# Optimization experiments

Hardware: AMD Instinct MI355X
Metric: run time of the kernel (lower is better)

The kernel has to match this reference:

```python
import jax, jax.numpy as jnp
import numpy as np

N_NODES = 200_000
N_UND = 3_200_000        # undirected masked edges
E = 2 * N_UND            # directed edges


def _seg_mean(m, dst, n_nodes):
    # DGL fn.mean: mean over incoming edge messages; zero-in-degree nodes get 0.
    s = jax.ops.segment_sum(m, dst, num_segments=n_nodes)
    deg = jax.ops.segment_sum(jnp.ones((m.shape[0], 1), m.dtype), dst, num_segments=n_nodes)
    return s / jnp.maximum(deg, 1.0)


def setup_inputs() -> dict:
    key = jax.random.key(0)
    ks = jax.random.split(key, 18)
    w = lambda k, s: jax.random.normal(k, s, dtype=jnp.float32) * 0.1
    return {
        'node_feat': jax.random.normal(ks[0], (N_NODES, 7), dtype=jnp.float32),
        'edge_feat': jax.random.normal(ks[1], (E, 4), dtype=jnp.float32),
        'edge_mask': jax.random.normal(ks[2], (N_UND, 1), dtype=jnp.float32),
        'src': jax.random.randint(ks[3], (E,), 0, N_NODES),
        'dst': jax.random.randint(ks[4], (E,), 0, N_NODES),
        'W1a': w(ks[5], (11, 32)), 'b1a': jnp.zeros((32,), jnp.float32),
        'W1b': w(ks[6], (32, 32)), 'b1b': jnp.zeros((32,), jnp.float32),
        'W2a': w(ks[7], (32, 32)), 'b2a': jnp.zeros((32,), jnp.float32),
        'W2b': w(ks[8], (32, 32)), 'b2b': jnp.zeros((32,), jnp.float32),
        'Wm1': w(ks[9], (32, 16)), 'bm1': jnp.zeros((16,), jnp.float32),
        'Wm2': w(ks[10], (16, 2)), 'bm2': jnp.zeros((2,), jnp.float32),
    }


def reference(node_feat, edge_feat, edge_mask, src, dst,
              W1a, b1a, W1b, b1b, W2a, b2a, W2b, b2b, Wm1, bm1, Wm2, bm2):
    n_nodes = node_feat.shape[0]
    relu = jax.nn.relu
    # interleave mask to both edge directions: [m0, m0, m1, m1, ...]
    m_full = jax.nn.sigmoid(jnp.repeat(edge_mask, 2, axis=0))  # [E, 1]
    # layer 1: masked cat(edge_h, src_h) -> mean over dst -> MLP
    msg1 = m_full * jnp.concatenate([edge_feat, node_feat[src]], axis=1)  # [E, 11]
    h = _seg_mean(msg1, dst, n_nodes)                                      # [N, 11]
    h = relu(relu(h @ W1a + b1a) @ W1b + b1b)                              # [N, 32]
    # layer 2: masked src_h -> mean over dst -> MLP
    msg2 = m_full * h[src]                                                 # [E, 32]
    h = _seg_mean(msg2, dst, n_nodes)                                      # [N, 32]
    h = relu(relu(h @ W2a + b2a) @ W2b + b2b)                              # [N, 32]
    # global max pool + readout MLP + softmax (batch_size=1 path)
    g = jnp.max(h, axis=0)                                                 # [32]
    logits = relu(g @ Wm1 + bm1) @ Wm2 + bm2                               # [2]
    return jax.nn.softmax(logits)[None, :]                                 # [1, 2]
```

## Files before the change

kernel.cpp:

```cpp
#include <hip/hip_runtime.h>
#include <hip/hip_fp16.h>
#include <math.h>

#define SCHUNK 1024
#define PMAX   80
#define BSHIFT 9
#define MAXBKT 1024
#define BINB   1024
#define EPT    8

__device__ __forceinline__ float sigmoidf_(float x) {
    return 1.0f / (1.0f + __expf(-x));
}

union I2H { int i; __half2 h; };
__device__ __forceinline__ int pack_h2(float a, float b) {
    I2H u; u.h = __floats2half2_rn(a, b); return u.i;
}
__device__ __forceinline__ float2 unpack_h2(int w) {
    I2H u; u.i = w; return __half22float2(u.h);
}

typedef int v4i_nt __attribute__((ext_vector_type(4)));
typedef float v4f_nt __attribute__((ext_vector_type(4)));
__device__ __forceinline__ int4 ldnt16(const int4* p) {
    v4i_nt v = __builtin_nontemporal_load((const v4i_nt*)p);
    return make_int4(v[0], v[1], v[2], v[3]);
}
__device__ __forceinline__ float4 ldnt16f(const float* p) {
    v4f_nt v = __builtin_nontemporal_load((const v4f_nt*)p);
    return make_float4(v[0], v[1], v[2], v[3]);
}

__global__ void hist_rank(const int* __restrict__ dst, int* __restrict__ deg,
                          int* __restrict__ rank, int E) {
    int e = blockIdx.x * blockDim.x + threadIdx.x;
    if (e < E) rank[e] = atomicAdd(&deg[dst[e]], 1);
}

__global__ void scan_part(const int* __restrict__ deg, int* __restrict__ bsum, int N) {
    __shared__ int tot[256];
    int t = threadIdx.x;
    int base = blockIdx.x * SCHUNK + t * 4;
    int s = 0;
    if (base + 3 < N) {
        int4 v = *(const int4*)(deg + base);
        s = v.x + v.y + v.z + v.w;
    } else {
#pragma unroll
        for (int j = 0; j < 4; ++j) if (base + j < N) s += deg[base + j];
    }
    tot[t] = s;
    __syncthreads();
    for (int o = 128; o >= 1; o >>= 1) {
        if (t < o) tot[t] += tot[t + o];
        __syncthreads();
    }
    if (t == 0) bsum[blockIdx.x] = tot[0];
}

__global__ void scan_mid(int* __restrict__ bsum, int* __restrict__ off, int B, int N) {
    __shared__ int tmp[256];
    int t = threadIdx.x;
    int chunk = (B + 255) / 256;
    int lo = t * chunk, hi = min(lo + chunk, B);
    int s = 0;
    for (int i = lo; i < hi; ++i) s += bsum[i];
    tmp[t] = s;
    __syncthreads();
    for (int o = 1; o < 256; o <<= 1) {
        int v = (t >= o) ? tmp[t - o] : 0;
        __syncthreads();
        tmp[t] += v;
        __syncthreads();
    }
    int run = (t == 0) ? 0 : tmp[t - 1];
    for (int i = lo; i < hi; ++i) { int d = bsum[i]; bsum[i] = run; run += d; }
    if (t == 255) off[N] = tmp[255];
}

__global__ void scan_fin(const int* __restrict__ deg, const int* __restrict__ bsum,
                         int* __restrict__ off, int N) {
    __shared__ int tots[256];
    int t = threadIdx.x;
    int base = blockIdx.x * SCHUNK + t * 4;
    int v0 = 0, v1 = 0, v2 = 0, v3 = 0;
    if (base + 3 < N) {
        int4 v = *(const int4*)(deg + base);
        v0 = v.x; v1 = v.y; v2 = v.z; v3 = v.w;
    } else {
        if (base + 0 < N) v0 = deg[base + 0];
        if (base + 1 < N) v1 = deg[base + 1];
        if (base + 2 < N) v2 = deg[base + 2];
        if (base + 3 < N) v3 = deg[base + 3];
    }
    tots[t] = v0 + v1 + v2 + v3;
    __syncthreads();
    for (int o = 1; o < 256; o <<= 1) {
        int v = (t >= o) ? tots[t - o] : 0;
        __syncthreads();
        tots[t] += v;
        __syncthreads();
    }
    int run = bsum[blockIdx.x] + ((t == 0) ? 0 : tots[t - 1]);
    if (base + 0 < N) off[base + 0] = run; run += v0;
    if (base + 1 < N) off[base + 1] = run; run += v1;
    if (base + 2 < N) off[base + 2] = run; run += v2;
    if (base + 3 < N) off[base + 3] = run;
}

__global__ void pack_nodes(const float* __restrict__ nf, int4* __restrict__ nf16, int N) {
    int n = blockIdx.x * blockDim.x + threadIdx.x;
    if (n >= N) return;
    const float* p = nf + (size_t)n * 7;
    int4 w;
    w.x = pack_h2(p[0], p[1]);
    w.y = pack_h2(p[2], p[3]);
    w.z = pack_h2(p[4], p[5]);
    w.w = pack_h2(p[6], 0.0f);
    nf16[n] = w;
}

__global__ __launch_bounds__(BINB)
void binA(const int* __restrict__ dst, const int* __restrict__ src,
          const float* __restrict__ edge_mask, const float* __restrict__ edge_feat,
          const float* __restrict__ node_feat,
          int* __restrict__ bktCnt, int4* __restrict__ region, int4* __restrict__ nf16,
          int E, int N, int nbkt, int bcap) {
    __shared__ int cnt[MAXBKT];
    __shared__ int base[MAXBKT];
    int t = threadIdx.x;
    int gt = blockIdx.x * BINB + t;
    if (gt < N) {
        const float* p = node_feat + (size_t)gt * 7;
        int4 w;
        w.x = pack_h2(p[0], p[1]);
        w.y = pack_h2(p[2], p[3]);
        w.z = pack_h2(p[4], p[5]);
        w.w = pack_h2(p[6], 0.0f);
        nf16[gt] = w;
    }
    for (int i = t; i < nbkt; i += BINB) cnt[i] = 0;
    __syncthreads();
    int4 rec[EPT];
    int  bl[EPT];
    int e0 = blockIdx.x * (BINB * EPT) + t;
#pragma unroll
    for (int j = 0; j < EPT; ++j) {
        int e = e0 + j * BINB;
        bl[j] = -1;
        if (e < E) {
            int d = dst[e];
            int s = src[e];
            float m = sigmoidf_(edge_mask[e >> 1]);
            float4 ef = ldnt16f(edge_feat + (size_t)e * 4);
            int b = d >> BSHIFT;
            int dlo = d & ((1 << BSHIFT) - 1);
            int lr = atomicAdd(&cnt[b], 1);
            rec[j].x = (dlo << 18) | s;
            rec[j].y = pack_h2(m * ef.x, m * ef.y);
            rec[j].z = pack_h2(m * ef.z, m * ef.w);
            rec[j].w = __float_as_int(m);
            bl[j] = (b << 16) | lr;
        }
    }
    __syncthreads();
    for (int i = t; i < nbkt; i += BINB)
        base[i] = atomicAdd(&bktCnt[i], cnt[i]);
    __syncthreads();
#pragma unroll
    for (int j = 0; j < EPT; ++j) {
        if (bl[j] >= 0) {
            int b = bl[j] >> 16, lr = bl[j] & 0xffff;
            int pos = base[b] + lr;
            if (pos < bcap) region[(size_t)b * bcap + pos] = rec[j];
        }
    }
}

__global__ __launch_bounds__(1024)
void fillS(const int4* __restrict__ region, const int* __restrict__ bktCnt,
           int4* __restrict__ recP, int* __restrict__ deg, int N, int bcap) {
    __shared__ int cnt[1 << BSHIFT];
    int b = blockIdx.x;
    int t = threadIdx.x;
    if (t < (1 << BSHIFT)) cnt[t] = 0;
    __syncthreads();
    int count = min(bktCnt[b], bcap);
    const int4* reg = region + (size_t)b * bcap;
    int n0 = b << BSHIFT;
    for (int i = t; i < count; i += blockDim.x) {
        int4 w = ldnt16(reg + i);
        int dlo = ((unsigned)w.x) >> 18;
        int r = atomicAdd(&cnt[dlo], 1);
        if (r < PMAX) {
            w.x &= 0x3FFFF;
            recP[(size_t)(n0 + dlo) * PMAX + r] = w;
        }
    }
    __syncthreads();
    if (t < (1 << BSHIFT) && n0 + t < N) deg[n0 + t] = cnt[t];
}

__global__ void hist_fill_p(const int* __restrict__ dst, const int* __restrict__ src,
                            const float* __restrict__ edge_mask,
                            const float* __restrict__ edge_feat,
                            const float* __restrict__ node_feat,
                            int* __restrict__ deg, int4* __restrict__ recP,
                            int4* __restrict__ nf16, int E, int N) {
    int t = blockIdx.x * blockDim.x + threadIdx.x;
    if (t < N) {
        const float* p = node_feat + (size_t)t * 7;
        int4 w;
        w.x = pack_h2(p[0], p[1]);
        w.y = pack_h2(p[2], p[3]);
        w.z = pack_h2(p[4], p[5]);
        w.w = pack_h2(p[6], 0.0f);
        nf16[t] = w;
    }
    int e0 = blockIdx.x * (blockDim.x << 2) + threadIdx.x;
    int e1 = e0 + blockDim.x;
    int e2 = e1 + blockDim.x;
    int e3 = e2 + blockDim.x;
    bool v0 = e0 < E, v1 = e1 < E, v2 = e2 < E, v3 = e3 < E;
    int d0 = 0, d1 = 0, d2 = 0, d3 = 0;
    int s0 = 0, s1 = 0, s2 = 0, s3 = 0;
    float k0 = 0, k1 = 0, k2 = 0, k3 = 0;
    float4 f0 = {}, f1 = {}, f2 = {}, f3 = {};
    if (v0) { d0 = dst[e0]; s0 = src[e0]; k0 = edge_mask[e0 >> 1]; f0 = ldnt16f(edge_feat + (size_t)e0 * 4); }
    if (v1) { d1 = dst[e1]; s1 = src[e1]; k1 = edge_mask[e1 >> 1]; f1 = ldnt16f(edge_feat + (size_t)e1 * 4); }
    if (v2) { d2 = dst[e2]; s2 = src[e2]; k2 = edge_mask[e2 >> 1]; f2 = ldnt16f(edge_feat + (size_t)e2 * 4); }
    if (v3) { d3 = dst[e3]; s3 = src[e3]; k3 = edge_mask[e3 >> 1]; f3 = ldnt16f(edge_feat + (size_t)e3 * 4); }
    float m0 = sigmoidf_(k0), m1 = sigmoidf_(k1), m2 = sigmoidf_(k2), m3 = sigmoidf_(k3);
    int4 w0, w1, w2, w3;
    w0.x = s0; w0.y = pack_h2(m0 * f0.x, m0 * f0.y); w0.z = pack_h2(m0 * f0.z, m0 * f0.w); w0.w = __float_as_int(m0);
    w1.x = s1; w1.y = pack_h2(m1 * f1.x, m1 * f1.y); w1.z = pack_h2(m1 * f1.z, m1 * f1.w); w1.w = __float_as_int(m1);
    w2.x = s2; w2.y = pack_h2(m2 * f2.x, m2 * f2.y); w2.z = pack_h2(m2 * f2.z, m2 * f2.w); w2.w = __float_as_int(m2);
    w3.x = s3; w3.y = pack_h2(m3 * f3.x, m3 * f3.y); w3.z = pack_h2(m3 * f3.z, m3 * f3.w); w3.w = __float_as_int(m3);
    int r0 = 0, r1 = 0, r2 = 0, r3 = 0;
    if (v0) r0 = atomicAdd(&deg[d0], 1);
    if (v1) r1 = atomicAdd(&deg[d1], 1);
    if (v2) r2 = atomicAdd(&deg[d2], 1);
    if (v3) r3 = atomicAdd(&deg[d3], 1);
    if (v0 && r0 < PMAX) recP[(size_t)d0 * PMAX + r0] = w0;
    if (v1 && r1 < PMAX) recP[(size_t)d1 * PMAX + r1] = w1;
    if (v2 && r2 < PMAX) recP[(size_t)d2 * PMAX + r2] = w2;
    if (v3 && r3 < PMAX) recP[(size_t)d3 * PMAX + r3] = w3;
}

__global__ void agg1_p(const int4* __restrict__ recP, const int* __restrict__ degv,
                       const int4* __restrict__ nf16,
                       const float* __restrict__ W1a, const float* __restrict__ b1a,
                       const float* __restrict__ W1b, const float* __restrict__ b1b,
                       __half* __restrict__ h1h, int N) {
    __shared__ float sW1a[11 * 32], sb1a[32], sW1b[32 * 32], sb1b[32];
    for (int i = threadIdx.x; i < 11 * 32; i += blockDim.x) sW1a[i] = W1a[i];
    for (int i = threadIdx.x; i < 32 * 32; i += blockDim.x) sW1b[i] = W1b[i];
    if (threadIdx.x < 32) { sb1a[threadIdx.x] = b1a[threadIdx.x]; sb1b[threadIdx.x] = b1b[threadIdx.x]; }
    __syncthreads();
    int n = blockIdx.x * (blockDim.x >> 2) + (threadIdx.x >> 2);
    int sub = threadIdx.x & 3;
    int deg = 0;
    size_t start = 0;
    if (n < N) { deg = degv[n]; start = (size_t)n * PMAX; }
    int dd = min(deg, PMAX);
    float x[11];
#pragma unroll
    for (int j = 0; j < 11; ++j) x[j] = 0.0f;
    int i = sub;
    for (; i + 4 < dd; i += 8) {
        int4 r0 = ldnt16(recP + start + i);
        int4 r1 = ldnt16(recP + start + i + 4);
        int4 nw0 = nf16[r0.x];
        int4 nw1 = nf16[r1.x];
        {
            float m = __int_as_float(r0.w);
            float2 e01 = unpack_h2(r0.y), e23 = unpack_h2(r0.z);
            x[0] += e01.x; x[1] += e01.y; x[2] += e23.x; x[3] += e23.y;
            float2 n01 = unpack_h2(nw0.x), n23 = unpack_h2(nw0.y);
            float2 n45 = unpack_h2(nw0.z), n6 = unpack_h2(nw0.w);
            x[4] += m * n01.x; x[5]  += m * n01.y; x[6] += m * n23.x; x[7] += m * n23.y;
            x[8] += m * n45.x; x[9]  += m * n45.y; x[10] += m * n6.x;
        }
        {
            float m = __int_as_float(r1.w);
            float2 e01 = unpack_h2(r1.y), e23 = unpack_h2(r1.z);
            x[0] += e01.x; x[1] += e01.y; x[2] += e23.x; x[3] += e23.y;
            float2 n01 = unpack_h2(nw1.x), n23 = unpack_h2(nw1.y);
            float2 n45 = unpack_h2(nw1.z), n6 = unpack_h2(nw1.w);
            x[4] += m * n01.x; x[5]  += m * n01.y; x[6] += m * n23.x; x[7] += m * n23.y;
            x[8] += m * n45.x; x[9]  += m * n45.y; x[10] += m * n6.x;
        }
    }
    for (; i < dd; i += 4) {
        int4 r = ldnt16(recP + start + i);
        float m = __int_as_float(r.w);
        float2 e01 = unpack_h2(r.y), e23 = unpack_h2(r.z);
        x[0] += e01.x; x[1] += e01.y; x[2] += e23.x; x[3] += e23.y;
        int4 nw = nf16[r.x];
        float2 n01 = unpack_h2(nw.x), n23 = unpack_h2(nw.y);
        float2 n45 = unpack_h2(nw.z), n6 = unpack_h2(nw.w);
        x[4] += m * n01.x; x[5]  += m * n01.y; x[6] += m * n23.x; x[7] += m * n23.y;
        x[8] += m * n45.x; x[9]  += m * n45.y; x[10] += m * n6.x;
    }
#pragma unroll
    for (int j = 0; j < 11; ++j) {
        x[j] += __shfl_xor(x[j], 1);
        x[j] += __shfl_xor(x[j], 2);
    }
    if (n >= N) return;
    float inv = 1.0f / fmaxf((float)deg, 1.0f);
#pragma unroll
    for (int j = 0; j < 11; ++j) x[j] *= inv;
    float hdn[32];
#pragma unroll
    for (int k = 0; k < 32; ++k) {
        float acc = sb1a[k];
#pragma unroll
        for (int j = 0; j < 11; ++j) acc += x[j] * sW1a[j * 32 + k];
        hdn[k] = fmaxf(acc, 0.0f);
    }
    float o[32];
#pragma unroll
    for (int k2 = 0; k2 < 32; ++k2) {
        float acc = sb1b[k2];
#pragma unroll
        for (int k = 0; k < 32; ++k) acc += hdn[k] * sW1b[k * 32 + k2];
        o[k2] = fmaxf(acc, 0.0f);
    }
    int4 w;
    w.x = pack_h2(o[8 * sub + 0], o[8 * sub + 1]);
    w.y = pack_h2(o[8 * sub + 2], o[8 * sub + 3]);
    w.z = pack_h2(o[8 * sub + 4], o[8 * sub + 5]);
    w.w = pack_h2(o[8 * sub + 6], o[8 * sub + 7]);
    ((int4*)(h1h + (size_t)n * 32))[sub] = w;
}

__global__ void agg2_p(const int4* __restrict__ recP, const int* __restrict__ degv,
                       const __half* __restrict__ h1h,
                       const float* __restrict__ W2a, const float* __restrict__ b2a,
                       const float* __restrict__ W2b, const float* __restrict__ b2b,
                       float* __restrict__ gmax, int N) {
    __shared__ float sW2a[32 * 32], sb2a[32], sW2b[32 * 32], sb2b[32];
    __shared__ int smax[32];
    for (int i = threadIdx.x; i < 32 * 32; i += blockDim.x) { sW2a[i] = W2a[i]; sW2b[i] = W2b[i]; }
    if (threadIdx.x < 32) {
        sb2a[threadIdx.x] = b2a[threadIdx.x];
        sb2b[threadIdx.x] = b2b[threadIdx.x];
        smax[threadIdx.x] = 0;
    }
    __syncthreads();
    int n = blockIdx.x * (blockDim.x >> 2) + (threadIdx.x >> 2);
    int sub = threadIdx.x & 3;
    bool valid = (n < N);
    int deg = 0;
    size_t start = 0;
    if (valid) { deg = degv[n]; start = (size_t)n * PMAX; }
    int dd = min(deg, PMAX);
    float x[32];
#pragma unroll
    for (int j = 0; j < 32; ++j) x[j] = 0.0f;
    int i = sub;
    for (; i + 4 < dd; i += 8) {
        int4 r0 = ldnt16(recP + start + i);
        int4 r1 = ldnt16(recP + start + i + 4);
        const int4* hp0 = (const int4*)(h1h + (size_t)r0.x * 32);
        const int4* hp1 = (const int4*)(h1h + (size_t)r1.x * 32);
        int4 g00 = hp0[0], g01 = hp0[1], g02 = hp0[2], g03 = hp0[3];
        int4 g10 = hp1[0], g11 = hp1[1], g12 = hp1[2], g13 = hp1[3];
        {
            float m = __int_as_float(r0.w);
            float2 a, b, c, d;
            a = unpack_h2(g00.x); b = unpack_h2(g00.y); c = unpack_h2(g00.z); d = unpack_h2(g00.w);
            x[0] += m * a.x; x[1] += m * a.y; x[2] += m * b.x; x[3] += m * b.y;
            x[4] += m * c.x; x[5] += m * c.y; x[6] += m * d.x; x[7] += m * d.y;
            a = unpack_h2(g01.x); b = unpack_h2(g01.y); c = unpack_h2(g01.z); d = unpack_h2(g01.w);
            x[8] += m * a.x; x[9] += m * a.y; x[10] += m * b.x; x[11] += m * b.y;
            x[12] += m * c.x; x[13] += m * c.y; x[14] += m * d.x; x[15] += m * d.y;
            a = unpack_h2(g02.x); b = unpack_h2(g02.y); c = unpack_h2(g02.z); d = unpack_h2(g02.w);
            x[16] += m * a.x; x[17] += m * a.y; x[18] += m * b.x; x[19] += m * b.y;
            x[20] += m * c.x; x[21] += m * c.y; x[22] += m * d.x; x[23] += m * d.y;
            a = unpack_h2(g03.x); b = unpack_h2(g03.y); c = unpack_h2(g03.z); d = unpack_h2(g03.w);
            x[24] += m * a.x; x[25] += m * a.y; x[26] += m * b.x; x[27] += m * b.y;
            x[28] += m * c.x; x[29] += m * c.y; x[30] += m * d.x; x[31] += m * d.y;
        }
        {
            float m = __int_as_float(r1.w);
            float2 a, b, c, d;
            a = unpack_h2(g10.x); b = unpack_h2(g10.y); c = unpack_h2(g10.z); d = unpack_h2(g10.w);
            x[0] += m * a.x; x[1] += m * a.y; x[2] += m * b.x; x[3] += m * b.y;
            x[4] += m * c.x; x[5] += m * c.y; x[6] += m * d.x; x[7] += m * d.y;
            a = unpack_h2(g11.x); b = unpack_h2(g11.y); c = unpack_h2(g11.z); d = unpack_h2(g11.w);
            x[8] += m * a.x; x[9] += m * a.y; x[10] += m * b.x; x[11] += m * b.y;
            x[12] += m * c.x; x[13] += m * c.y; x[14] += m * d.x; x[15] += m * d.y;
            a = unpack_h2(g12.x); b = unpack_h2(g12.y); c = unpack_h2(g12.z); d = unpack_h2(g12.w);
            x[16] += m * a.x; x[17] += m * a.y; x[18] += m * b.x; x[19] += m * b.y;
            x[20] += m * c.x; x[21] += m * c.y; x[22] += m * d.x; x[23] += m * d.y;
            a = unpack_h2(g13.x); b = unpack_h2(g13.y); c = unpack_h2(g13.z); d = unpack_h2(g13.w);
            x[24] += m * a.x; x[25] += m * a.y; x[26] += m * b.x; x[27] += m * b.y;
            x[28] += m * c.x; x[29] += m * c.y; x[30] += m * d.x; x[31] += m * d.y;
        }
    }
    for (; i < dd; i += 4) {
        int4 r = ldnt16(recP + start + i);
        float m = __int_as_float(r.w);
        const int4* hp = (const int4*)(h1h + (size_t)r.x * 32);
#pragma unroll
        for (int q = 0; q < 4; ++q) {
            int4 v = hp[q];
            float2 a = unpack_h2(v.x), b = unpack_h2(v.y);
            float2 c = unpack_h2(v.z), d = unpack_h2(v.w);
            x[8 * q + 0] += m * a.x; x[8 * q + 1] += m * a.y;
            x[8 * q + 2] += m * b.x; x[8 * q + 3] += m * b.y;
            x[8 * q + 4] += m * c.x; x[8 * q + 5] += m * c.y;
            x[8 * q + 6] += m * d.x; x[8 * q + 7] += m * d.y;
        }
    }
#pragma unroll
    for (int j = 0; j < 32; ++j) {
        x[j] += __shfl_xor(x[j], 1);
        x[j] += __shfl_xor(x[j], 2);
    }
    float inv = 1.0f / fmaxf((float)deg, 1.0f);
#pragma unroll
    for (int j = 0; j < 32; ++j) x[j] *= inv;
    float hdn[32];
#pragma unroll
    for (int k = 0; k < 32; ++k) {
        float acc = sb2a[k];
#pragma unroll
        for (int j = 0; j < 32; ++j) acc += x[j] * sW2a[j * 32 + k];
        hdn[k] = fmaxf(acc, 0.0f);
    }
    int lane = threadIdx.x & 63;
#pragma unroll
    for (int k2 = 0; k2 < 32; ++k2) {
        float acc = sb2b[k2];
#pragma unroll
        for (int k = 0; k < 32; ++k) acc += hdn[k] * sW2b[k * 32 + k2];
        float v = valid ? fmaxf(acc, 0.0f) : 0.0f;
#pragma unroll
        for (int o = 32; o >= 1; o >>= 1)
            v = fmaxf(v, __shfl_xor(v, o));
        if (lane == 0) atomicMax(&smax[k2], __float_as_int(v));
    }
    __syncthreads();
    if (threadIdx.x < 32) atomicMax((int*)&gmax[threadIdx.x], smax[threadIdx.x]);
}

__global__ void fill_rec16(const int* __restrict__ dst, const int* __restrict__ rank,
                           const int* __restrict__ off,
                           const float* __restrict__ edge_mask,
                           const int* __restrict__ src,
                           const float* __restrict__ edge_feat,
                           int4* __restrict__ rec, int E) {
    int e = blockIdx.x * blockDim.x + threadIdx.x;
    if (e >= E) return;
    int p = off[dst[e]] + rank[e];
    float m = sigmoidf_(edge_mask[e >> 1]);
    float4 ef = ldnt16f(edge_feat + (size_t)e * 4);
    int4 w;
    w.x = src[e];
    w.y = pack_h2(m * ef.x, m * ef.y);
    w.z = pack_h2(m * ef.z, m * ef.w);
    w.w = __float_as_int(m);
    rec[p] = w;
}

__global__ void agg1_16(const int4* __restrict__ rec, const int* __restrict__ off,
                        const int4* __restrict__ nf16,
                        const float* __restrict__ W1a, const float* __restrict__ b1a,
                        const float* __restrict__ W1b, const float* __restrict__ b1b,
                        __half* __restrict__ h1h, int N) {
    __shared__ float sW1a[11 * 32], sb1a[32], sW1b[32 * 32], sb1b[32];
    for (int i = threadIdx.x; i < 11 * 32; i += blockDim.x) sW1a[i] = W1a[i];
    for (int i = threadIdx.x; i < 32 * 32; i += blockDim.x) sW1b[i] = W1b[i];
    if (threadIdx.x < 32) { sb1a[threadIdx.x] = b1a[threadIdx.x]; sb1b[threadIdx.x] = b1b[threadIdx.x]; }
    __syncthreads();
    int n = blockIdx.x * (blockDim.x >> 2) + (threadIdx.x >> 2);
    int sub = threadIdx.x & 3;
    int start = 0, deg = 0;
    if (n < N) { start = off[n]; deg = off[n + 1] - start; }
    float x[11];
#pragma unroll
    for (int j = 0; j < 11; ++j) x[j] = 0.0f;
    for (int i = sub; i < deg; i += 4) {
        int4 r = ldnt16(rec + start + i);
        float m = __int_as_float(r.w);
        float2 e01 = unpack_h2(r.y), e23 = unpack_h2(r.z);
        x[0] += e01.x; x[1] += e01.y; x[2] += e23.x; x[3] += e23.y;
        int4 nw = nf16[r.x];
        float2 n01 = unpack_h2(nw.x), n23 = unpack_h2(nw.y);
        float2 n45 = unpack_h2(nw.z), n6 = unpack_h2(nw.w);
        x[4] += m * n01.x; x[5]  += m * n01.y; x[6] += m * n23.x; x[7] += m * n23.y;
        x[8] += m * n45.x; x[9]  += m * n45.y; x[10] += m * n6.x;
    }
#pragma unroll
    for (int j = 0; j < 11; ++j) {
        x[j] += __shfl_xor(x[j], 1);
        x[j] += __shfl_xor(x[j], 2);
    }
    if (n >= N) return;
    float inv = 1.0f / fmaxf((float)deg, 1.0f);
#pragma unroll
    for (int j = 0; j < 11; ++j) x[j] *= inv;
    float hdn[32];
#pragma unroll
    for (int k = 0; k < 32; ++k) {
        float acc = sb1a[k];
#pragma unroll
        for (int j = 0; j < 11; ++j) acc += x[j] * sW1a[j * 32 + k];
        hdn[k] = fmaxf(acc, 0.0f);
    }
    float o[32];
#pragma unroll
    for (int k2 = 0; k2 < 32; ++k2) {
        float acc = sb1b[k2];
#pragma unroll
        for (int k = 0; k < 32; ++k) acc += hdn[k] * sW1b[k * 32 + k2];
        o[k2] = fmaxf(acc, 0.0f);
    }
    int4 w;
    w.x = pack_h2(o[8 * sub + 0], o[8 * sub + 1]);
    w.y = pack_h2(o[8 * sub + 2], o[8 * sub + 3]);
    w.z = pack_h2(o[8 * sub + 4], o[8 * sub + 5]);
    w.w = pack_h2(o[8 * sub + 6], o[8 * sub + 7]);
    ((int4*)(h1h + (size_t)n * 32))[sub] = w;
}

__global__ void agg2_16(const int4* __restrict__ rec, const int* __restrict__ off,
                        const __half* __restrict__ h1h,
                        const float* __restrict__ W2a, const float* __restrict__ b2a,
                        const float* __restrict__ W2b, const float* __restrict__ b2b,
                        float* __restrict__ gmax, int N) {
    __shared__ float sW2a[32 * 32], sb2a[32], sW2b[32 * 32], sb2b[32];
    __shared__ int smax[32];
    for (int i = threadIdx.x; i < 32 * 32; i += blockDim.x) { sW2a[i] = W2a[i]; sW2b[i] = W2b[i]; }
    if (threadIdx.x < 32) {
        sb2a[threadIdx.x] = b2a[threadIdx.x];
        sb2b[threadIdx.x] = b2b[threadIdx.x];
        smax[threadIdx.x] = 0;
    }
    __syncthreads();
    int n = blockIdx.x * (blockDim.x >> 2) + (threadIdx.x >> 2);
    int sub = threadIdx.x & 3;
    bool valid = (n < N);
    int start = 0, deg = 0;
    if (valid) { start = off[n]; deg = off[n + 1] - start; }
    float x[32];
#pragma unroll
    for (int j = 0; j < 32; ++j) x[j] = 0.0f;
    for (int i = sub; i < deg; i += 4) {
        int4 r = ldnt16(rec + start + i);
        float m = __int_as_float(r.w);
        const int4* hp = (const int4*)(h1h + (size_t)r.x * 32);
#pragma unroll
        for (int q = 0; q < 4; ++q) {
            int4 v = hp[q];
            float2 a = unpack_h2(v.x), b = unpack_h2(v.y);
            float2 c = unpack_h2(v.z), d = unpack_h2(v.w);
            x[8 * q + 0] += m * a.x; x[8 * q + 1] += m * a.y;
            x[8 * q + 2] += m * b.x; x[8 * q + 3] += m * b.y;
            x[8 * q + 4] += m * c.x; x[8 * q + 5] += m * c.y;
            x[8 * q + 6] += m * d.x; x[8 * q + 7] += m * d.y;
        }
    }
#pragma unroll
    for (int j = 0; j < 32; ++j) {
        x[j] += __shfl_xor(x[j], 1);
        x[j] += __shfl_xor(x[j], 2);
    }
    float inv = 1.0f / fmaxf((float)deg, 1.0f);
#pragma unroll
    for (int j = 0; j < 32; ++j) x[j] *= inv;
    float hdn[32];
#pragma unroll
    for (int k = 0; k < 32; ++k) {
        float acc = sb2a[k];
#pragma unroll
        for (int j = 0; j < 32; ++j) acc += x[j] * sW2a[j * 32 + k];
        hdn[k] = fmaxf(acc, 0.0f);
    }
    int lane = threadIdx.x & 63;
#pragma unroll
    for (int k2 = 0; k2 < 32; ++k2) {
        float acc = sb2b[k2];
#pragma unroll
        for (int k = 0; k < 32; ++k) acc += hdn[k] * sW2b[k * 32 + k2];
        float v = valid ? fmaxf(acc, 0.0f) : 0.0f;
#pragma unroll
        for (int o = 32; o >= 1; o >>= 1)
            v = fmaxf(v, __shfl_xor(v, o));
        if (lane == 0) atomicMax(&smax[k2], __float_as_int(v));
    }
    __syncthreads();
    if (threadIdx.x < 32) atomicMax((int*)&gmax[threadIdx.x], smax[threadIdx.x]);
}

__global__ void fill_rec(const int* __restrict__ dst, const int* __restrict__ rank,
                         const int* __restrict__ off,
                         const float* __restrict__ edge_mask,
                         const int* __restrict__ src,
                         int2* __restrict__ rec, int E) {
    int e = blockIdx.x * blockDim.x + threadIdx.x;
    if (e >= E) return;
    int p = off[dst[e]] + rank[e];
    float m = sigmoidf_(edge_mask[e >> 1]);
    int mq = (int)(m * 16384.0f + 0.5f);
    mq = min(mq, 16383);
    unsigned packed = ((unsigned)src[e] << 14) | (unsigned)mq;
    rec[p] = make_int2(e, (int)packed);
}

__global__ void agg1_rec(const int2* __restrict__ rec, const int* __restrict__ off,
                         const float* __restrict__ edge_feat,
                         const float* __restrict__ node_feat,
                         const float* __restrict__ W1a, const float* __restrict__ b1a,
                         const float* __restrict__ W1b, const float* __restrict__ b1b,
                         float* __restrict__ h1, int N) {
    __shared__ float sW1a[11 * 32], sb1a[32], sW1b[32 * 32], sb1b[32];
    for (int i = threadIdx.x; i < 11 * 32; i += blockDim.x) sW1a[i] = W1a[i];
    for (int i = threadIdx.x; i < 32 * 32; i += blockDim.x) sW1b[i] = W1b[i];
    if (threadIdx.x < 32) { sb1a[threadIdx.x] = b1a[threadIdx.x]; sb1b[threadIdx.x] = b1b[threadIdx.x]; }
    __syncthreads();
    int n = blockIdx.x * blockDim.x + threadIdx.x;
    if (n >= N) return;
    int start = off[n];
    int deg = off[n + 1] - start;
    float x[11];
#pragma unroll
    for (int j = 0; j < 11; ++j) x[j] = 0.0f;
    for (int i = 0; i < deg; ++i) {
        int2 r = rec[start + i];
        int e = r.x;
        unsigned packed = (unsigned)r.y;
        int s = (int)(packed >> 14);
        float m = (float)(packed & 16383u) * (1.0f / 16384.0f);
        float4 ef = *(const float4*)(edge_feat + (size_t)e * 4);
        x[0] += m * ef.x; x[1] += m * ef.y; x[2] += m * ef.z; x[3] += m * ef.w;
        const float* nf = node_feat + (size_t)s * 7;
#pragma unroll
        for (int j = 0; j < 7; ++j) x[4 + j] += m * nf[j];
    }
    float inv = 1.0f / fmaxf((float)deg, 1.0f);
#pragma unroll
    for (int j = 0; j < 11; ++j) x[j] *= inv;
    float hdn[32];
#pragma unroll
    for (int k = 0; k < 32; ++k) {
        float acc = sb1a[k];
#pragma unroll
        for (int j = 0; j < 11; ++j) acc += x[j] * sW1a[j * 32 + k];
        hdn[k] = fmaxf(acc, 0.0f);
    }
    float o[32];
#pragma unroll
    for (int k2 = 0; k2 < 32; ++k2) {
        float acc = sb1b[k2];
#pragma unroll
        for (int k = 0; k < 32; ++k) acc += hdn[k] * sW1b[k * 32 + k2];
        o[k2] = fmaxf(acc, 0.0f);
    }
    float4* outp = (float4*)(h1 + (size_t)n * 32);
#pragma unroll
    for (int q = 0; q < 8; ++q)
        outp[q] = make_float4(o[4 * q], o[4 * q + 1], o[4 * q + 2], o[4 * q + 3]);
}

__global__ void agg2_rec(const int2* __restrict__ rec, const int* __restrict__ off,
                         const float* __restrict__ h1,
                         const float* __restrict__ W2a, const float* __restrict__ b2a,
                         const float* __restrict__ W2b, const float* __restrict__ b2b,
                         float* __restrict__ gmax, int N) {
    __shared__ float sW2a[32 * 32], sb2a[32], sW2b[32 * 32], sb2b[32];
    __shared__ int smax[32];
    for (int i = threadIdx.x; i < 32 * 32; i += blockDim.x) { sW2a[i] = W2a[i]; sW2b[i] = W2b[i]; }
    if (threadIdx.x < 32) {
        sb2a[threadIdx.x] = b2a[threadIdx.x];
        sb2b[threadIdx.x] = b2b[threadIdx.x];
        smax[threadIdx.x] = 0;
    }
    __syncthreads();
    int n = blockIdx.x * blockDim.x + threadIdx.x;
    bool valid = (n < N);
    int nn = valid ? n : 0;
    int start = valid ? off[nn] : 0;
    int deg = valid ? (off[nn + 1] - start) : 0;
    float x[32];
#pragma unroll
    for (int j = 0; j < 32; ++j) x[j] = 0.0f;
    for (int i = 0; i < deg; ++i) {
        int2 r = rec[start + i];
        unsigned packed = (unsigned)r.y;
        int s = (int)(packed >> 14);
        float m = (float)(packed & 16383u) * (1.0f / 16384.0f);
        const float4* hp = (const float4*)(h1 + (size_t)s * 32);
#pragma unroll
        for (int q = 0; q < 8; ++q) {
            float4 v = hp[q];
            x[4 * q + 0] += m * v.x;
            x[4 * q + 1] += m * v.y;
            x[4 * q + 2] += m * v.z;
            x[4 * q + 3] += m * v.w;
        }
    }
    float inv = 1.0f / fmaxf((float)deg, 1.0f);
#pragma unroll
    for (int j = 0; j < 32; ++j) x[j] *= inv;
    float hdn[32];
#pragma unroll
    for (int k = 0; k < 32; ++k) {
        float acc = sb2a[k];
#pragma unroll
        for (int j = 0; j < 32; ++j) acc += x[j] * sW2a[j * 32 + k];
        hdn[k] = fmaxf(acc, 0.0f);
    }
    int lane = threadIdx.x & 63;
#pragma unroll
    for (int k2 = 0; k2 < 32; ++k2) {
        float acc = sb2b[k2];
#pragma unroll
        for (int k = 0; k < 32; ++k) acc += hdn[k] * sW2b[k * 32 + k2];
        float v = valid ? fmaxf(acc, 0.0f) : 0.0f;
#pragma unroll
        for (int o = 32; o >= 1; o >>= 1)
            v = fmaxf(v, __shfl_xor(v, o));
        if (lane == 0) atomicMax(&smax[k2], __float_as_int(v));
    }
    __syncthreads();
    if (threadIdx.x < 32) atomicMax((int*)&gmax[threadIdx.x], smax[threadIdx.x]);
}

__global__ void readout(const float* __restrict__ gmax,
                        const float* __restrict__ Wm1, const float* __restrict__ bm1,
                        const float* __restrict__ Wm2, const float* __restrict__ bm2,
                        float* __restrict__ out) {
    __shared__ float p[16];
    int t = threadIdx.x;
    if (t < 16) {
        float acc = bm1[t];
        for (int j = 0; j < 32; ++j) acc += gmax[j] * Wm1[j * 16 + t];
        p[t] = fmaxf(acc, 0.0f);
    }
    __syncthreads();
    if (t == 0) {
        float l0 = bm2[0], l1 = bm2[1];
        for (int k = 0; k < 16; ++k) { l0 += p[k] * Wm2[k * 2]; l1 += p[k] * Wm2[k * 2 + 1]; }
        float mx = fmaxf(l0, l1);
        float e0 = __expf(l0 - mx), e1 = __expf(l1 - mx);
        float s = e0 + e1;
        out[0] = e0 / s;
        out[1] = e1 / s;
    }
}

static inline size_t align16(size_t x) { return (x + 15) & ~(size_t)15; }

extern "C" void kernel_launch(void* const* d_in, const int* in_sizes, int n_in,
                              void* d_out, int out_size, void* d_ws, size_t ws_size,
                              hipStream_t stream) {
    const float* node_feat = (const float*)d_in[0];
    const float* edge_feat = (const float*)d_in[1];
    const float* edge_mask = (const float*)d_in[2];
    const int*   src       = (const int*)d_in[3];
    const int*   dst       = (const int*)d_in[4];
    const float* W1a = (const float*)d_in[5];
    const float* b1a = (const float*)d_in[6];
    const float* W1b = (const float*)d_in[7];
    const float* b1b = (const float*)d_in[8];
    const float* W2a = (const float*)d_in[9];
    const float* b2a = (const float*)d_in[10];
    const float* W2b = (const float*)d_in[11];
    const float* b2b = (const float*)d_in[12];
    const float* Wm1 = (const float*)d_in[13];
    const float* bm1 = (const float*)d_in[14];
    const float* Wm2 = (const float*)d_in[15];
    const float* bm2 = (const float*)d_in[16];

    const int N = in_sizes[0] / 7;
    const int E = in_sizes[3];
    const int B = (N + SCHUNK - 1) / SCHUNK;

    {
        const int nbkt = (N + (1 << BSHIFT) - 1) >> BSHIFT;
        if (nbkt <= MAXBKT && N <= (1 << 18)) {
            int avg = (E + nbkt - 1) / nbkt;
            int bcap = avg + avg / 8 + 256;
            char* basep = (char*)d_ws;
            size_t off0 = 0;
            int*   bktCnt = (int*)(basep + off0);  off0 += (size_t)(nbkt + 32) * sizeof(int);
            float* gmax   = (float*)(bktCnt + nbkt);
            off0 = align16(off0);
            int*   degS   = (int*)(basep + off0);  off0 += (size_t)N * sizeof(int);
            off0 = align16(off0);
            int4*  nf16   = (int4*)(basep + off0); off0 += (size_t)N * sizeof(int4);
            int4*  recP   = (int4*)(basep + off0); off0 += (size_t)N * PMAX * sizeof(int4);
            int4*  region = (int4*)(basep + off0);
            __half* h1h   = (__half*)region;
            size_t regionBytes = (size_t)nbkt * bcap * sizeof(int4);
            size_t h1Bytes = (size_t)N * 32 * sizeof(__half);
            off0 += (regionBytes > h1Bytes ? regionBytes : h1Bytes);
            const size_t needS = off0;
            if (ws_size >= needS) {
                hipMemsetAsync(d_ws, 0, (size_t)(nbkt + 32) * sizeof(int), stream);
                const int binBlocks = (max(E, N) + BINB * EPT - 1) / (BINB * EPT);
                binA<<<binBlocks, BINB, 0, stream>>>(dst, src, edge_mask, edge_feat, node_feat,
                                                     bktCnt, region, nf16, E, N, nbkt, bcap);
                fillS<<<nbkt, 1024, 0, stream>>>(region, bktCnt, recP, degS, N, bcap);
                const int nodeBlocks = (N + 63) / 64;
                agg1_p<<<nodeBlocks, 256, 0, stream>>>(recP, degS, nf16,
                                                       W1a, b1a, W1b, b1b, h1h, N);
                agg2_p<<<nodeBlocks, 256, 0, stream>>>(recP, degS, h1h,
                                                       W2a, b2a, W2b, b2b, gmax, N);
                readout<<<1, 64, 0, stream>>>(gmax, Wm1, bm1, Wm2, bm2, (float*)d_out);
                return;
            }
        }
    }

    {
        int*    deg_i = (int*)d_ws;
        float*  gmax  = (float*)(deg_i + N);
        __half* h1h   = (__half*)(gmax + 32);
        int4*   nf16  = (int4*)(h1h + (size_t)N * 32);
        int4*   recP  = nf16 + N;
        const size_t needP = (size_t)(deg_i + N + 32 - (int*)d_ws) * sizeof(int)
                           + (size_t)N * 32 * sizeof(__half)
                           + (size_t)N * sizeof(int4)
                           + (size_t)N * PMAX * sizeof(int4);
        if (ws_size >= needP) {
            hipMemsetAsync(d_ws, 0, (size_t)(N + 32) * sizeof(int), stream);
            int threadsNeeded = max((E + 3) / 4, N);
            const int gridEF = (threadsNeeded + 255) / 256;
            hist_fill_p<<<gridEF, 256, 0, stream>>>(dst, src, edge_mask, edge_feat,
                                                    node_feat, deg_i, recP, nf16, E, N);
            const int nodeBlocks = (N + 63) / 64;
            agg1_p<<<nodeBlocks, 256, 0, stream>>>(recP, deg_i, nf16,
                                                   W1a, b1a, W1b, b1b, h1h, N);
            agg2_p<<<nodeBlocks, 256, 0, stream>>>(recP, deg_i, h1h,
                                                   W2a, b2a, W2b, b2b, gmax, N);
            readout<<<1, 64, 0, stream>>>(gmax, Wm1, bm1, Wm2, bm2, (float*)d_out);
            return;
        }
    }

    int*   deg_i = (int*)d_ws;
    float* gmax  = (float*)(deg_i + N);
    int*   off   = (int*)(gmax + 32);
    int*   bsum  = off + (N + 1);
    int*   slot  = bsum + (B + 1);

    const size_t slot16 = (size_t)E > (size_t)16 * N ? (size_t)E : (size_t)16 * N;
    int*    rank   = slot;
    __half* h1h    = (__half*)slot;
    int4*   rec16  = (int4*)(slot + slot16);
    int4*   nf16   = rec16 + E;
    const size_t need16 = ((size_t)2 * N + 34 + B + slot16 + (size_t)E * 4 + (size_t)N * 4) * sizeof(int);

    const size_t slot8 = (size_t)E > (size_t)32 * N ? (size_t)E : (size_t)32 * N;
    float* h1f  = (float*)slot;
    int2*  rec8 = (int2*)(slot + slot8);

    hipMemsetAsync(d_ws, 0, (size_t)(N + 32) * sizeof(int), stream);

    hist_rank<<<(E + 255) / 256, 256, 0, stream>>>(dst, deg_i, rank, E);
    scan_part<<<B, 256, 0, stream>>>(deg_i, bsum, N);
    scan_mid<<<1, 256, 0, stream>>>(bsum, off, B, N);
    scan_fin<<<B, 256, 0, stream>>>(deg_i, bsum, off, N);

    if (ws_size >= need16) {
        const int nodeBlocks = (N + 63) / 64;
        pack_nodes<<<(N + 255) / 256, 256, 0, stream>>>(node_feat, nf16, N);
        fill_rec16<<<(E + 255) / 256, 256, 0, stream>>>(dst, rank, off, edge_mask, src,
                                                        edge_feat, rec16, E);
        agg1_16<<<nodeBlocks, 256, 0, stream>>>(rec16, off, nf16,
                                                W1a, b1a, W1b, b1b, h1h, N);
        agg2_16<<<nodeBlocks, 256, 0, stream>>>(rec16, off, h1h,
                                                W2a, b2a, W2b, b2b, gmax, N);
    } else {
        fill_rec<<<(E + 255) / 256, 256, 0, stream>>>(dst, rank, off, edge_mask, src, rec8, E);
        agg1_rec<<<(N + 255) / 256, 256, 0, stream>>>(rec8, off, edge_feat, node_feat,
                                                      W1a, b1a, W1b, b1b, h1f, N);
        agg2_rec<<<(N + 255) / 256, 256, 0, stream>>>(rec8, off, h1f,
                                                      W2a, b2a, W2b, b2b, gmax, N);
    }
    readout<<<1, 64, 0, stream>>>(gmax, Wm1, bm1, Wm2, bm2, (float*)d_out);
}
```

Baseline: 668.3 us.

## Sort per-node edge records by source tile in bucket fill kernel

fillS now runs two passes over each bucket. The first builds a per-destination histogram keyed by source tile (src>>14) and prefix-sums it. The second scatters records so each node's incoming edges are grouped by source range, aiming to make the later gathers of node features and h1 rows more cache-local. The cost is a second read of the bucket region and a larger shared histogram. The unused fallback fp16 CSR path is also removed.

```diff
diff --git a/kernel.cpp b/kernel.cpp
--- a/kernel.cpp
+++ b/kernel.cpp
@@ -5,9 +5,12 @@
 #define SCHUNK 1024
 #define PMAX   80
 #define BSHIFT 9
+#define RB     (1 << BSHIFT)
 #define MAXBKT 1024
 #define BINB   1024
 #define EPT    8
+#define TSHIFT 14
+#define TDIM   16
 
 __device__ __forceinline__ float sigmoidf_(float x) {
     return 1.0f / (1.0f + __expf(-x));
@@ -155,7 +158,7 @@
             float m = sigmoidf_(edge_mask[e >> 1]);
             float4 ef = ldnt16f(edge_feat + (size_t)e * 4);
             int b = d >> BSHIFT;
-            int dlo = d & ((1 << BSHIFT) - 1);
+            int dlo = d & (RB - 1);
             int lr = atomicAdd(&cnt[b], 1);
             rec[j].x = (dlo << 18) | s;
             rec[j].y = pack_h2(m * ef.x, m * ef.y);
@@ -181,25 +184,43 @@
 __global__ __launch_bounds__(1024)
 void fillS(const int4* __restrict__ region, const int* __restrict__ bktCnt,
            int4* __restrict__ recP, int* __restrict__ deg, int N, int bcap) {
-    __shared__ int cnt[1 << BSHIFT];
+    __shared__ int cnt[RB * TDIM];
     int b = blockIdx.x;
     int t = threadIdx.x;
-    if (t < (1 << BSHIFT)) cnt[t] = 0;
+    for (int i = t; i < RB * TDIM; i += blockDim.x) cnt[i] = 0;
     __syncthreads();
     int count = min(bktCnt[b], bcap);
     const int4* reg = region + (size_t)b * bcap;
     int n0 = b << BSHIFT;
     for (int i = t; i < count; i += blockDim.x) {
+        int wx = reg[i].x;
+        int dlo = ((unsigned)wx) >> 18;
+        int tile = (wx & 0x3FFFF) >> TSHIFT;
+        atomicAdd(&cnt[dlo * TDIM + tile], 1);
+    }
+    __syncthreads();
+    if (t < RB) {
+        int run = 0;
+#pragma unroll
+        for (int k = 0; k < TDIM; ++k) {
+            int c = cnt[t * TDIM + k];
+            cnt[t * TDIM + k] = run;
+            run += c;
+        }
+        if (n0 + t < N) deg[n0 + t] = run;
+    }
+    __syncthreads();
+    for (int i = t; i < count; i += blockDim.x) {
         int4 w = ldnt16(reg + i);
         int dlo = ((unsigned)w.x) >> 18;
-        int r = atomicAdd(&cnt[dlo], 1);
-        if (r < PMAX) {
-            w.x &= 0x3FFFF;
-            recP[(size_t)(n0 + dlo) * PMAX + r] = w;
-        }
-    }
-    __syncthreads();
-    if (t < (1 << BSHIFT) && n0 + t < N) deg[n0 + t] = cnt[t];
+        int s = w.x & 0x3FFFF;
+        int tile = s >> TSHIFT;
+        int slot = atomicAdd(&cnt[dlo * TDIM + tile], 1);
+        if (slot < PMAX) {
+            w.x = s;
+            recP[(size_t)(n0 + dlo) * PMAX + slot] = w;
+        }
+    }
 }
 
 __global__ void hist_fill_p(const int* __restrict__ dst, const int* __restrict__ src,
@@ -448,155 +469,6 @@
     if (threadIdx.x < 32) atomicMax((int*)&gmax[threadIdx.x], smax[threadIdx.x]);
 }
 
-__global__ void fill_rec16(const int* __restrict__ dst, const int* __restrict__ rank,
-                           const int* __restrict__ off,
-                           const float* __restrict__ edge_mask,
-                           const int* __restrict__ src,
-                           const float* __restrict__ edge_feat,
-                           int4* __restrict__ rec, int E) {
-    int e = blockIdx.x * blockDim.x + threadIdx.x;
-    if (e >= E) return;
-    int p = off[dst[e]] + rank[e];
-    float m = sigmoidf_(edge_mask[e >> 1]);
-    float4 ef = ldnt16f(edge_feat + (size_t)e * 4);
-    int4 w;
-    w.x = src[e];
-    w.y = pack_h2(m * ef.x, m * ef.y);
-    w.z = pack_h2(m * ef.z, m * ef.w);
-    w.w = __float_as_int(m);
-    rec[p] = w;
-}
-
-__global__ void agg1_16(const int4* __restrict__ rec, const int* __restrict__ off,
-                        const int4* __restrict__ nf16,
-                        const float* __restrict__ W1a, const float* __restrict__ b1a,
-                        const float* __restrict__ W1b, const float* __restrict__ b1b,
-                        __half* __restrict__ h1h, int N) {
-    __shared__ float sW1a[11 * 32], sb1a[32], sW1b[32 * 32], sb1b[32];
-    for (int i = threadIdx.x; i < 11 * 32; i += blockDim.x) sW1a[i] = W1a[i];
-    for (int i = threadIdx.x; i < 32 * 32; i += blockDim.x) sW1b[i] = W1b[i];
-    if (threadIdx.x < 32) { sb1a[threadIdx.x] = b1a[threadIdx.x]; sb1b[threadIdx.x] = b1b[threadIdx.x]; }
-    __syncthreads();
-    int n = blockIdx.x * (blockDim.x >> 2) + (threadIdx.x >> 2);
-    int sub = threadIdx.x & 3;
-    int start = 0, deg = 0;
-    if (n < N) { start = off[n]; deg = off[n + 1] - start; }
-    float x[11];
-#pragma unroll
-    for (int j = 0; j < 11; ++j) x[j] = 0.0f;
-    for (int i = sub; i < deg; i += 4) {
-        int4 r = ldnt16(rec + start + i);
-        float m = __int_as_float(r.w);
-        float2 e01 = unpack_h2(r.y), e23 = unpack_h2(r.z);
-        x[0] += e01.x; x[1] += e01.y; x[2] += e23.x; x[3] += e23.y;
-        int4 nw = nf16[r.x];
-        float2 n01 = unpack_h2(nw.x), n23 = unpack_h2(nw.y);
-        float2 n45 = unpack_h2(nw.z), n6 = unpack_h2(nw.w);
-        x[4] += m * n01.x; x[5]  += m * n01.y; x[6] += m * n23.x; x[7] += m * n23.y;
-        x[8] += m * n45.x; x[9]  += m * n45.y; x[10] += m * n6.x;
-    }
-#pragma unroll
-    for (int j = 0; j < 11; ++j) {
-        x[j] += __shfl_xor(x[j], 1);
-        x[j] += __shfl_xor(x[j], 2);
-    }
-    if (n >= N) return;
-    float inv = 1.0f / fmaxf((float)deg, 1.0f);
-#pragma unroll
-    for (int j = 0; j < 11; ++j) x[j] *= inv;
-    float hdn[32];
-#pragma unroll
-    for (int k = 0; k < 32; ++k) {
-        float acc = sb1a[k];
-#pragma unroll
-        for (int j = 0; j < 11; ++j) acc += x[j] * sW1a[j * 32 + k];
-        hdn[k] = fmaxf(acc, 0.0f);
-    }
-    float o[32];
-#pragma unroll
-    for (int k2 = 0; k2 < 32; ++k2) {
-        float acc = sb1b[k2];
-#pragma unroll
-        for (int k = 0; k < 32; ++k) acc += hdn[k] * sW1b[k * 32 + k2];
-        o[k2] = fmaxf(acc, 0.0f);
-    }
-    int4 w;
-    w.x = pack_h2(o[8 * sub + 0], o[8 * sub + 1]);
-    w.y = pack_h2(o[8 * sub + 2], o[8 * sub + 3]);
-    w.z = pack_h2(o[8 * sub + 4], o[8 * sub + 5]);
-    w.w = pack_h2(o[8 * sub + 6], o[8 * sub + 7]);
-    ((int4*)(h1h + (size_t)n * 32))[sub] = w;
-}
-
-__global__ void agg2_16(const int4* __restrict__ rec, const int* __restrict__ off,
-                        const __half* __restrict__ h1h,
-                        const float* __restrict__ W2a, const float* __restrict__ b2a,
-                        const float* __restrict__ W2b, const float* __restrict__ b2b,
-                        float* __restrict__ gmax, int N) {
-    __shared__ float sW2a[32 * 32], sb2a[32], sW2b[32 * 32], sb2b[32];
-    __shared__ int smax[32];
-    for (int i = threadIdx.x; i < 32 * 32; i += blockDim.x) { sW2a[i] = W2a[i]; sW2b[i] = W2b[i]; }
-    if (threadIdx.x < 32) {
-        sb2a[threadIdx.x] = b2a[threadIdx.x];
-        sb2b[threadIdx.x] = b2b[threadIdx.x];
-        smax[threadIdx.x] = 0;
-    }
-    __syncthreads();
-    int n = blockIdx.x * (blockDim.x >> 2) + (threadIdx.x >> 2);
-    int sub = threadIdx.x & 3;
-    bool valid = (n < N);
-    int start = 0, deg = 0;
-    if (valid) { start = off[n]; deg = off[n + 1] - start; }
-    float x[32];
-#pragma unroll
-    for (int j = 0; j < 32; ++j) x[j] = 0.0f;
-    for (int i = sub; i < deg; i += 4) {
-        int4 r = ldnt16(rec + start + i);
-        float m = __int_as_float(r.w);
-        const int4* hp = (const int4*)(h1h + (size_t)r.x * 32);
-#pragma unroll
-        for (int q = 0; q < 4; ++q) {
-            int4 v = hp[q];
-            float2 a = unpack_h2(v.x), b = unpack_h2(v.y);
-            float2 c = unpack_h2(v.z), d = unpack_h2(v.w);
-            x[8 * q + 0] += m * a.x; x[8 * q + 1] += m * a.y;
-            x[8 * q + 2] += m * b.x; x[8 * q + 3] += m * b.y;
-            x[8 * q + 4] += m * c.x; x[8 * q + 5] += m * c.y;
-            x[8 * q + 6] += m * d.x; x[8 * q + 7] += m * d.y;
-        }
-    }
-#pragma unroll
-    for (int j = 0; j < 32; ++j) {
-        x[j] += __shfl_xor(x[j], 1);
-        x[j] += __shfl_xor(x[j], 2);
-    }
-    float inv = 1.0f / fmaxf((float)deg, 1.0f);
-#pragma unroll
-    for (int j = 0; j < 32; ++j) x[j] *= inv;
-    float hdn[32];
-#pragma unroll
-    for (int k = 0; k < 32; ++k) {
-        float acc = sb2a[k];
-#pragma unroll
-        for (int j = 0; j < 32; ++j) acc += x[j] * sW2a[j * 32 + k];
-        hdn[k] = fmaxf(acc, 0.0f);
-    }
-    int lane = threadIdx.x & 63;
-#pragma unroll
-    for (int k2 = 0; k2 < 32; ++k2) {
-        float acc = sb2b[k2];
-#pragma unroll
-        for (int k = 0; k < 32; ++k) acc += hdn[k] * sW2b[k * 32 + k2];
-        float v = valid ? fmaxf(acc, 0.0f) : 0.0f;
-#pragma unroll
-        for (int o = 32; o >= 1; o >>= 1)
-            v = fmaxf(v, __shfl_xor(v, o));
-        if (lane == 0) atomicMax(&smax[k2], __float_as_int(v));
-    }
-    __syncthreads();
-    if (threadIdx.x < 32) atomicMax((int*)&gmax[threadIdx.x], smax[threadIdx.x]);
-}
-
 __global__ void fill_rec(const int* __restrict__ dst, const int* __restrict__ rank,
                          const int* __restrict__ off,
                          const float* __restrict__ edge_mask,
@@ -782,7 +654,7 @@
     const int B = (N + SCHUNK - 1) / SCHUNK;
 
     {
-        const int nbkt = (N + (1 << BSHIFT) - 1) >> BSHIFT;
+        const int nbkt = (N + RB - 1) >> BSHIFT;
         if (nbkt <= MAXBKT && N <= (1 << 18)) {
             int avg = (E + nbkt - 1) / nbkt;
             int bcap = avg + avg / 8 + 256;
@@ -849,40 +721,20 @@
     int*   off   = (int*)(gmax + 32);
     int*   bsum  = off + (N + 1);
     int*   slot  = bsum + (B + 1);
-
-    const size_t slot16 = (size_t)E > (size_t)16 * N ? (size_t)E : (size_t)16 * N;
-    int*    rank   = slot;
-    __half* h1h    = (__half*)slot;
-    int4*   rec16  = (int4*)(slot + slot16);
-    int4*   nf16   = rec16 + E;
-    const size_t need16 = ((size_t)2 * N + 34 + B + slot16 + (size_t)E * 4 + (size_t)N * 4) * sizeof(int);
-
     const size_t slot8 = (size_t)E > (size_t)32 * N ? (size_t)E : (size_t)32 * N;
+    int*   rank = slot;
     float* h1f  = (float*)slot;
     int2*  rec8 = (int2*)(slot + slot8);
 
     hipMemsetAsync(d_ws, 0, (size_t)(N + 32) * sizeof(int), stream);
-
     hist_rank<<<(E + 255) / 256, 256, 0, stream>>>(dst, deg_i, rank, E);
     scan_part<<<B, 256, 0, stream>>>(deg_i, bsum, N);
     scan_mid<<<1, 256, 0, stream>>>(bsum, off, B, N);
     scan_fin<<<B, 256, 0, stream>>>(deg_i, bsum, off, N);
-
-    if (ws_size >= need16) {
-        const int nodeBlocks = (N + 63) / 64;
-        pack_nodes<<<(N + 255) / 256, 256, 0, stream>>>(node_feat, nf16, N);
-        fill_rec16<<<(E + 255) / 256, 256, 0, stream>>>(dst, rank, off, edge_mask, src,
-                                                        edge_feat, rec16, E);
-        agg1_16<<<nodeBlocks, 256, 0, stream>>>(rec16, off, nf16,
-                                                W1a, b1a, W1b, b1b, h1h, N);
-        agg2_16<<<nodeBlocks, 256, 0, stream>>>(rec16, off, h1h,
-                                                W2a, b2a, W2b, b2b, gmax, N);
-    } else {
-        fill_rec<<<(E + 255) / 256, 256, 0, stream>>>(dst, rank, off, edge_mask, src, rec8, E);
-        agg1_rec<<<(N + 255) / 256, 256, 0, stream>>>(rec8, off, edge_feat, node_feat,
-                                                      W1a, b1a, W1b, b1b, h1f, N);
-        agg2_rec<<<(N + 255) / 256, 256, 0, stream>>>(rec8, off, h1f,
-                                                      W2a, b2a, W2b, b2b, gmax, N);
-    }
+    fill_rec<<<(E + 255) / 256, 256, 0, stream>>>(dst, rank, off, edge_mask, src, rec8, E);
+    agg1_rec<<<(N + 255) / 256, 256, 0, stream>>>(rec8, off, edge_feat, node_feat,
+                                                  W1a, b1a, W1b, b1b, h1f, N);
+    agg2_rec<<<(N + 255) / 256, 256, 0, stream>>>(rec8, off, h1f,
+                                                  W2a, b2a, W2b, b2b, gmax, N);
     readout<<<1, 64, 0, stream>>>(gmax, Wm1, bm1, Wm2, bm2, (float*)d_out);
 }
```

Measured after the change: 721.9 us. 8.0% more time.
